# Optimization experiments

Measured on AMD Instinct MI355X. Metric: run time of the kernel, lower is better.

Reference implementation:

```python
import jax, jax.numpy as jnp
import numpy as np

B = 128          # batch
M_SIZE = 32      # mps bond dimension (init kwarg mps_size)
NQ = 16          # num_qubits -> 2**16 basis states


def setup_inputs() -> dict:
    key = jax.random.key(0)
    ks = jax.random.split(key, 4)
    def lin(k, out_d, in_d):
        return jax.random.normal(k, (out_d, in_d), jnp.float32) * (1.0 / np.sqrt(in_d))
    mat = M_SIZE * M_SIZE
    return {
        "x": jax.random.normal(ks[0], (B, 4), jnp.float32),
        "W1": lin(ks[1], 1024, 4),        "b1": jnp.zeros((1024,), jnp.float32),
        "W2": lin(ks[2], 32, 1024),       "b2": jnp.zeros((32,), jnp.float32),
        "W3": lin(ks[3], 2 * mat, 32),    "b3": jnp.zeros((2 * mat,), jnp.float32),
        "num_qubits": NQ,
    }


def _chain_products(M, k):
    """M: [2, B, m, m] site matrices (index 0 = spin_up, 1 = spin_down).
    Returns [2**k, B, m, m]: matrix products A_{s1} @ ... @ A_{sk} for every
    length-k bit string s, ordered as ascending binary (MSB = first/leftmost site),
    matching seq_gen's enumeration order."""
    arr = M
    for _ in range(k - 1):  # recursive doubling over sites (static small loop)
        arr = jnp.einsum('sbij,tbjk->stbik', arr, M)
        arr = arr.reshape((-1,) + M.shape[1:])
    return arr


def reference(x, W1, b1, W2, b2, W3, b3, num_qubits):
    # Encoder MLP (dropout is identity in eval mode)
    h = jax.nn.relu(x @ W1.T + b1)
    h = jax.nn.relu(h @ W2.T + b2)
    e = h @ W3.T + b3                         # [B, 2*m*m]
    m = int(np.sqrt(e.shape[-1] // 2))
    # view(-1, 2, m, m); split dim=1 -> spin_up = [:,0], spin_down = [:,1]
    Ms = e.reshape(-1, 2, m, m).transpose(1, 0, 2, 3)   # [2, B, m, m]
    # Decode: coeff(state) = trace(prod of site matrices). Split the chain in
    # two halves; trace(L_s @ R_t) = sum_ij L[s,i,j] * R[t,j,i].
    k1 = num_qubits // 2
    k2 = num_qubits - k1
    L = _chain_products(Ms, k1)               # [2^k1, B, m, m]
    R = _chain_products(Ms, k2)               # [2^k2, B, m, m]
    coeffs = jnp.einsum('sbij,tbji->stb', L, R)   # [2^k1, 2^k2, B]
    gs = coeffs.reshape(-1, coeffs.shape[-1]).T   # [B, 2^n], binary-ascending order
    return gs / jnp.linalg.norm(gs, axis=1, keepdims=True)
```

## Files before the change

kernel.cpp:

```cpp
#include <hip/hip_runtime.h>
#include <hip/hip_bf16.h>
#include <math.h>

#define BDIM 128

typedef short sh8 __attribute__((ext_vector_type(8)));
typedef __bf16 bf8 __attribute__((ext_vector_type(8)));
typedef float f32x4 __attribute__((ext_vector_type(4)));

__device__ inline float bf2f(unsigned short u) {
    union { unsigned int i; float f; } v; v.i = ((unsigned int)u) << 16; return v.f;
}
__device__ inline unsigned short f2bf(float f) {
    union { unsigned int i; float f; } v; v.f = f;
    unsigned int x = v.i;
    return (unsigned short)((x + 0x7FFFu + ((x >> 16) & 1u)) >> 16);
}

__device__ inline sh8 xshuf(sh8 v, int u) {
    switch (u & 7) {
    case 0: return v;
    case 1: return __builtin_shufflevector(v,v,1,0,3,2,5,4,7,6);
    case 2: return __builtin_shufflevector(v,v,2,3,0,1,6,7,4,5);
    case 3: return __builtin_shufflevector(v,v,3,2,1,0,7,6,5,4);
    case 4: return __builtin_shufflevector(v,v,4,5,6,7,0,1,2,3);
    case 5: return __builtin_shufflevector(v,v,5,4,7,6,1,0,3,2);
    case 6: return __builtin_shufflevector(v,v,6,7,4,5,2,3,0,1);
    default: return __builtin_shufflevector(v,v,7,6,5,4,3,2,1,0);
    }
}

__global__ __launch_bounds__(256) void mlp_kernel(
    const float* __restrict__ x,
    const float* __restrict__ W1, const float* __restrict__ b1,
    const float* __restrict__ W2, const float* __restrict__ b2,
    const float* __restrict__ W3, const float* __restrict__ b3,
    float* __restrict__ Mout)
{
    __shared__ float h1[1024];
    __shared__ float part[8][33];
    __shared__ float h2[32];
    int b = blockIdx.x, t = threadIdx.x;
    float x0 = x[b*4+0], x1 = x[b*4+1], x2 = x[b*4+2], x3 = x[b*4+3];
#pragma unroll
    for (int q = 0; q < 4; ++q) {
        int j = t + 256*q;
        float4 w = *(const float4*)(W1 + (size_t)j*4);
        float v = x0*w.x + x1*w.y + x2*w.z + x3*w.w + b1[j];
        h1[j] = v > 0.f ? v : 0.f;
    }
    __syncthreads();
    {
        int o = t & 31, chunk = t >> 5;
        const float* w2r = W2 + (size_t)o*1024 + chunk*128;
        const float* h1r = h1 + chunk*128;
        float s = 0.f;
#pragma unroll
        for (int k = 0; k < 128; k += 4) {
            float4 w = *(const float4*)(w2r + k);
            s += h1r[k]*w.x + h1r[k+1]*w.y + h1r[k+2]*w.z + h1r[k+3]*w.w;
        }
        part[chunk][o] = s;
    }
    __syncthreads();
    if (t < 32) {
        float s = b2[t];
#pragma unroll
        for (int c = 0; c < 8; ++c) s += part[c][t];
        h2[t] = s > 0.f ? s : 0.f;
    }
    __syncthreads();
#pragma unroll
    for (int q = 0; q < 8; ++q) {
        int j = t + 256*q;
        const float* w3r = W3 + (size_t)j*32;
        float s = b3[j];
#pragma unroll
        for (int i = 0; i < 32; i += 4) {
            float4 w = *(const float4*)(w3r + i);
            s += h2[i]*w.x + h2[i+1]*w.y + h2[i+2]*w.z + h2[i+3]*w.w;
        }
        Mout[(size_t)b*2048 + j] = s;
    }
}

__global__ __launch_bounds__(256) void small_chain(
    const float* __restrict__ Mb, float* __restrict__ P4n)
{
    int b = blockIdx.x, t = threadIdx.x;
    __shared__ float aT[2][32][36], an[2][32][36];
    __shared__ float p2T[4][32][36], p2n[4][32][36];
    int w = t >> 6, l = t & 63;
    {
        const float* src = Mb + (size_t)b*2048;
#pragma unroll
        for (int r = 0; r < 2; ++r) {
            int e = t*4 + r*1024;
            float4 v = *(const float4*)(src + e);
            int mat = e >> 10, off = e & 1023;
            int row = off >> 5, c = off & 31;
            *(float4*)&an[mat][row][c] = v;
            aT[mat][c+0][row] = v.x; aT[mat][c+1][row] = v.y;
            aT[mat][c+2][row] = v.z; aT[mat][c+3][row] = v.w;
        }
    }
    __syncthreads();
    int r0 = (l >> 3) << 2, c0 = (l & 7) << 2;
    {
        float acc[4][4] = {};
#pragma unroll 8
        for (int kk = 0; kk < 32; ++kk) {
            float a[4], bb[4];
            *(float4*)a  = *(const float4*)&aT[w>>1][kk][r0];
            *(float4*)bb = *(const float4*)&an[w&1][kk][c0];
#pragma unroll
            for (int i = 0; i < 4; ++i)
#pragma unroll
                for (int j = 0; j < 4; ++j)
                    acc[i][j] += a[i]*bb[j];
        }
#pragma unroll
        for (int i = 0; i < 4; ++i)
#pragma unroll
            for (int j = 0; j < 4; ++j) {
                p2n[w][r0+i][c0+j] = acc[i][j];
                p2T[w][c0+j][r0+i] = acc[i][j];
            }
    }
    __syncthreads();
#pragma unroll
    for (int it = 0; it < 4; ++it) {
        int u = (w << 2) | it;
        float acc[4][4] = {};
#pragma unroll 8
        for (int kk = 0; kk < 32; ++kk) {
            float a[4], bb[4];
            *(float4*)a  = *(const float4*)&p2T[w][kk][r0];
            *(float4*)bb = *(const float4*)&p2n[it][kk][c0];
#pragma unroll
            for (int i = 0; i < 4; ++i)
#pragma unroll
                for (int j = 0; j < 4; ++j)
                    acc[i][j] += a[i]*bb[j];
        }
        float* dst = P4n + ((size_t)b*16 + u)*1024;
#pragma unroll
        for (int i = 0; i < 4; ++i)
            *(float4*)(dst + (r0+i)*32 + c0) =
                make_float4(acc[i][0], acc[i][1], acc[i][2], acc[i][3]);
    }
}

__global__ __launch_bounds__(256) void ll_kernel(
    const float* __restrict__ P4n, unsigned short* __restrict__ LL)
{
    int b = blockIdx.y;
    int q0 = blockIdx.x * 4;
    int hi = q0 >> 4;
    __shared__ float parT[32][36];
    __shared__ float mm[4][32][36];
    __shared__ unsigned short stage[4][1024];
    int t = threadIdx.x, w = t >> 6, l = t & 63;
    {
        const float* src = P4n + ((size_t)b*16 + hi)*1024;
        int e = t*4;
        float4 v = *(const float4*)(src + e);
        int row = e >> 5, c = e & 31;
        parT[c+0][row] = v.x; parT[c+1][row] = v.y;
        parT[c+2][row] = v.z; parT[c+3][row] = v.w;
    }
    {
        const float* src = P4n + ((size_t)b*16 + ((q0 & 15) | w))*1024;
#pragma unroll
        for (int r = 0; r < 4; ++r) {
            int e = r*256 + l*4;
            *(float4*)&mm[w][e>>5][e&31] = *(const float4*)(src + e);
        }
    }
    __syncthreads();
    int r0 = (l >> 3) << 2, c0 = (l & 7) << 2;
    float acc[4][4] = {};
#pragma unroll 8
    for (int kk = 0; kk < 32; ++kk) {
        float a[4], bb[4];
        *(float4*)a  = *(const float4*)&parT[kk][r0];
        *(float4*)bb = *(const float4*)&mm[w][kk][c0];
#pragma unroll
        for (int i = 0; i < 4; ++i)
#pragma unroll
            for (int j = 0; j < 4; ++j)
                acc[i][j] += a[i]*bb[j];
    }
#pragma unroll
    for (int i = 0; i < 4; ++i)
#pragma unroll
        for (int j = 0; j < 4; ++j) {
            int r = r0 + i, c = c0 + j;
            stage[w][((r ^ c) << 5) | c] = f2bf(acc[i][j]);
        }
    __syncthreads();
    unsigned short* dst = LL + ((size_t)b*256 + q0)*1024;
    const uint4* s4 = (const uint4*)&stage[0][0];
    uint4* d4 = (uint4*)dst;
    d4[t] = s4[t];
    d4[t + 256] = s4[t + 256];
}

__global__ __launch_bounds__(256) void pair_gemm_mfma(
    const unsigned short* __restrict__ LL,
    float* __restrict__ out, float* __restrict__ norm2)
{
    int b = blockIdx.y;
    int ti = blockIdx.x >> 1, tj = blockIdx.x & 1;
    const unsigned short* Ab = LL + (size_t)b*262144 + (size_t)ti*131072;
    const unsigned short* Bb = LL + (size_t)b*262144 + (size_t)tj*131072;
    __shared__ __align__(16) unsigned short As[2][128][40];
    __shared__ __align__(16) unsigned short Bs[2][128][40];
    __shared__ float wsum[4];
    int t = threadIdx.x;
    int w = t >> 6, l = t & 63;
    int row0 = t >> 2;
    int j8 = (t & 3) * 8;
    int wm = (w >> 1) * 64, wn = (w & 1) * 64;
    int lr = l & 15, lg = l >> 4;

    const unsigned short* Ar0 = Ab + (size_t)row0*1024;
    const unsigned short* Ar1 = Ab + (size_t)(row0+64)*1024;
    const unsigned short* Br0 = Bb + (size_t)row0*1024;
    const unsigned short* Br1 = Bb + (size_t)(row0+64)*1024;

    f32x4 acc[4][4] = {};
    sh8 ra0, ra1, rb0, rb1;

    ra0 = *(const sh8*)(Ar0 + j8);
    ra1 = *(const sh8*)(Ar1 + j8);
    rb0 = *(const sh8*)(Br0 + j8);
    rb1 = *(const sh8*)(Br1 + j8);
    *(sh8*)&As[0][row0][j8]    = ra0;
    *(sh8*)&As[0][row0+64][j8] = ra1;
    *(sh8*)&Bs[0][row0][j8]    = rb0;
    *(sh8*)&Bs[0][row0+64][j8] = rb1;
    __syncthreads();

#pragma unroll
    for (int d = 0; d < 32; ++d) {
        int cur = d & 1, nxt = cur ^ 1;
        int dn = d + 1;
        if (dn < 32) {
            int aoff = dn*32 + j8;
            int boff = dn*32 + (j8 ^ ((dn >> 3) << 3));
            ra0 = *(const sh8*)(Ar0 + aoff);
            ra1 = *(const sh8*)(Ar1 + aoff);
            rb0 = *(const sh8*)(Br0 + boff);
            rb1 = *(const sh8*)(Br1 + boff);
        }
        bf8 av[4], bv[4];
#pragma unroll
        for (int m = 0; m < 4; ++m) {
            av[m] = __builtin_bit_cast(bf8, *(const sh8*)&As[cur][wm + m*16 + lr][lg*8]);
            bv[m] = __builtin_bit_cast(bf8, *(const sh8*)&Bs[cur][wn + m*16 + lr][lg*8]);
        }
#pragma unroll
        for (int m = 0; m < 4; ++m)
#pragma unroll
            for (int n = 0; n < 4; ++n)
                acc[m][n] = __builtin_amdgcn_mfma_f32_16x16x32_bf16(av[m], bv[n], acc[m][n], 0, 0, 0);
        if (dn < 32) {
            int u = dn & 7;
            *(sh8*)&As[nxt][row0][j8]    = ra0;
            *(sh8*)&As[nxt][row0+64][j8] = ra1;
            *(sh8*)&Bs[nxt][row0][j8]    = xshuf(rb0, u);
            *(sh8*)&Bs[nxt][row0+64][j8] = xshuf(rb1, u);
        }
        __syncthreads();
    }

    float ss = 0.f;
    size_t ob = (size_t)b*65536;
#pragma unroll
    for (int m = 0; m < 4; ++m) {
#pragma unroll
        for (int n = 0; n < 4; ++n) {
            f32x4 v = acc[m][n];
            int s0 = ti*128 + wm + m*16 + lg*4;
            int t0 = tj*128 + wn + n*16 + lr;
            float* op = out + ob + (size_t)s0*256 + t0;
#pragma unroll
            for (int r = 0; r < 4; ++r) {
                op[r*256] = v[r];
                ss += v[r]*v[r];
            }
        }
    }
#pragma unroll
    for (int o = 1; o < 64; o <<= 1) ss += __shfl_xor(ss, o);
    if (l == 0) wsum[w] = ss;
    __syncthreads();
    if (t == 0) atomicAdd(norm2 + b, wsum[0]+wsum[1]+wsum[2]+wsum[3]);
}

__global__ __launch_bounds__(256) void scale_kernel(
    float* __restrict__ out, const float* __restrict__ norm2)
{
    size_t i = (size_t)blockIdx.x * 256 + threadIdx.x;
    int b = (int)(i >> 14);
    float s = rsqrtf(norm2[b]);
    float4 v = ((const float4*)out)[i];
    v.x *= s; v.y *= s; v.z *= s; v.w *= s;
    ((float4*)out)[i] = v;
}

extern "C" void kernel_launch(void* const* d_in, const int* in_sizes, int n_in,
                              void* d_out, int out_size, void* d_ws, size_t ws_size,
                              hipStream_t stream)
{
    (void)in_sizes; (void)n_in;
    const float* x  = (const float*)d_in[0];
    const float* W1 = (const float*)d_in[1];
    const float* b1 = (const float*)d_in[2];
    const float* W2 = (const float*)d_in[3];
    const float* b2 = (const float*)d_in[4];
    const float* W3 = (const float*)d_in[5];
    const float* b3 = (const float*)d_in[6];
    float* out = (float*)d_out;

    char* W = (char*)d_ws;
    const size_t MB = 1024*1024;
    unsigned short* LL = (unsigned short*)(W + 0);
    float* P4 = (float*)(W + 64*MB);
    float* Mb = (float*)(W + 72*MB);
    float* nrm = (float*)(W + 73*MB);
    const size_t NEED = 73*MB + 512;
    if (ws_size < NEED) {
        hipMemsetAsync(d_out, 0, (size_t)out_size * sizeof(float), stream);
        return;
    }

    hipMemsetAsync(nrm, 0, BDIM*sizeof(float), stream);
    mlp_kernel<<<BDIM, 256, 0, stream>>>(x, W1, b1, W2, b2, W3, b3, Mb);
    small_chain<<<BDIM, 256, 0, stream>>>(Mb, P4);
    ll_kernel<<<dim3(64, BDIM), 256, 0, stream>>>(P4, LL);
    pair_gemm_mfma<<<dim3(4, BDIM), 256, 0, stream>>>(LL, out, nrm);
    scale_kernel<<<8192, 256, 0, stream>>>(out, nrm);
}
```

Baseline: 183.5 us.

## Fuse encoder with chain products and compute level-8 products via bf16 MFMA

Merges the MLP encoder and the 2/4-site chain product kernels into one kernel, keeping site matrices in shared memory and folding the norm memset into it. The 4-site products are written as bf16 in both normal and transposed layouts. The 8-site product stage is rewritten as a bf16 MFMA kernel in which each block computes 16 outputs instead of 4. This cuts launches and global round trips, but adds bf16 rounding one stage earlier, which may reduce accuracy.

```diff
diff --git a/kernel.cpp b/kernel.cpp
--- a/kernel.cpp
+++ b/kernel.cpp
@@ -30,17 +30,21 @@
     }
 }
 
-__global__ __launch_bounds__(256) void mlp_kernel(
+__global__ __launch_bounds__(256) void enc_fused(
     const float* __restrict__ x,
     const float* __restrict__ W1, const float* __restrict__ b1,
     const float* __restrict__ W2, const float* __restrict__ b2,
     const float* __restrict__ W3, const float* __restrict__ b3,
-    float* __restrict__ Mout)
+    unsigned short* __restrict__ P4n, unsigned short* __restrict__ P4t,
+    float* __restrict__ nrm)
 {
     __shared__ float h1[1024];
     __shared__ float part[8][33];
     __shared__ float h2[32];
+    __shared__ float aT[2][32][36], an[2][32][36];
+    __shared__ float p2T[4][32][36], p2n[4][32][36];
     int b = blockIdx.x, t = threadIdx.x;
+    if (t == 0) nrm[b] = 0.f;
     float x0 = x[b*4+0], x1 = x[b*4+1], x2 = x[b*4+2], x3 = x[b*4+3];
 #pragma unroll
     for (int q = 0; q < 4; ++q) {
@@ -80,31 +84,13 @@
             float4 w = *(const float4*)(w3r + i);
             s += h2[i]*w.x + h2[i+1]*w.y + h2[i+2]*w.z + h2[i+3]*w.w;
         }
-        Mout[(size_t)b*2048 + j] = s;
-    }
-}
-
-__global__ __launch_bounds__(256) void small_chain(
-    const float* __restrict__ Mb, float* __restrict__ P4n)
-{
-    int b = blockIdx.x, t = threadIdx.x;
-    __shared__ float aT[2][32][36], an[2][32][36];
-    __shared__ float p2T[4][32][36], p2n[4][32][36];
+        int spin = j >> 10, off = j & 1023;
+        int row = off >> 5, c = off & 31;
+        an[spin][row][c] = s;
+        aT[spin][c][row] = s;
+    }
+    __syncthreads();
     int w = t >> 6, l = t & 63;
-    {
-        const float* src = Mb + (size_t)b*2048;
-#pragma unroll
-        for (int r = 0; r < 2; ++r) {
-            int e = t*4 + r*1024;
-            float4 v = *(const float4*)(src + e);
-            int mat = e >> 10, off = e & 1023;
-            int row = off >> 5, c = off & 31;
-            *(float4*)&an[mat][row][c] = v;
-            aT[mat][c+0][row] = v.x; aT[mat][c+1][row] = v.y;
-            aT[mat][c+2][row] = v.z; aT[mat][c+3][row] = v.w;
-        }
-    }
-    __syncthreads();
     int r0 = (l >> 3) << 2, c0 = (l & 7) << 2;
     {
         float acc[4][4] = {};
@@ -143,67 +129,86 @@
                 for (int j = 0; j < 4; ++j)
                     acc[i][j] += a[i]*bb[j];
         }
-        float* dst = P4n + ((size_t)b*16 + u)*1024;
-#pragma unroll
-        for (int i = 0; i < 4; ++i)
-            *(float4*)(dst + (r0+i)*32 + c0) =
-                make_float4(acc[i][0], acc[i][1], acc[i][2], acc[i][3]);
-    }
-}
-
-__global__ __launch_bounds__(256) void ll_kernel(
-    const float* __restrict__ P4n, unsigned short* __restrict__ LL)
-{
-    int b = blockIdx.y;
-    int q0 = blockIdx.x * 4;
-    int hi = q0 >> 4;
-    __shared__ float parT[32][36];
-    __shared__ float mm[4][32][36];
-    __shared__ unsigned short stage[4][1024];
-    int t = threadIdx.x, w = t >> 6, l = t & 63;
+        unsigned short* dstN = P4n + ((size_t)b*16 + u)*1024;
+        unsigned short* dstT = P4t + ((size_t)b*16 + u)*1024;
+#pragma unroll
+        for (int i = 0; i < 4; ++i) {
+            ushort4 v; v.x = f2bf(acc[i][0]); v.y = f2bf(acc[i][1]);
+            v.z = f2bf(acc[i][2]); v.w = f2bf(acc[i][3]);
+            *(ushort4*)(dstN + (r0+i)*32 + c0) = v;
+        }
+#pragma unroll
+        for (int j = 0; j < 4; ++j) {
+            ushort4 v; v.x = f2bf(acc[0][j]); v.y = f2bf(acc[1][j]);
+            v.z = f2bf(acc[2][j]); v.w = f2bf(acc[3][j]);
+            *(ushort4*)(dstT + (c0+j)*32 + r0) = v;
+        }
+    }
+}
+
+__global__ __launch_bounds__(256) void ll_mfma(
+    const unsigned short* __restrict__ P4n, const unsigned short* __restrict__ P4t,
+    unsigned short* __restrict__ LL)
+{
+    int hi = blockIdx.x, b = blockIdx.y;
+    __shared__ __align__(16) unsigned short As[32][40];
+    __shared__ __align__(16) unsigned short Bs[512][40];
+    __shared__ __align__(16) unsigned short outst[16][1024];
+    int t = threadIdx.x;
+    int w = t >> 6, l = t & 63;
+    int lr = l & 15, lg = l >> 4;
+    int wn = w * 128;
+
     {
-        const float* src = P4n + ((size_t)b*16 + hi)*1024;
-        int e = t*4;
-        float4 v = *(const float4*)(src + e);
-        int row = e >> 5, c = e & 31;
-        parT[c+0][row] = v.x; parT[c+1][row] = v.y;
-        parT[c+2][row] = v.z; parT[c+3][row] = v.w;
-    }
-    {
-        const float* src = P4n + ((size_t)b*16 + ((q0 & 15) | w))*1024;
-#pragma unroll
-        for (int r = 0; r < 4; ++r) {
-            int e = r*256 + l*4;
-            *(float4*)&mm[w][e>>5][e&31] = *(const float4*)(src + e);
-        }
-    }
-    __syncthreads();
-    int r0 = (l >> 3) << 2, c0 = (l & 7) << 2;
-    float acc[4][4] = {};
-#pragma unroll 8
-    for (int kk = 0; kk < 32; ++kk) {
-        float a[4], bb[4];
-        *(float4*)a  = *(const float4*)&parT[kk][r0];
-        *(float4*)bb = *(const float4*)&mm[w][kk][c0];
-#pragma unroll
-        for (int i = 0; i < 4; ++i)
-#pragma unroll
-            for (int j = 0; j < 4; ++j)
-                acc[i][j] += a[i]*bb[j];
-    }
-#pragma unroll
-    for (int i = 0; i < 4; ++i)
-#pragma unroll
-        for (int j = 0; j < 4; ++j) {
-            int r = r0 + i, c = c0 + j;
-            stage[w][((r ^ c) << 5) | c] = f2bf(acc[i][j]);
-        }
-    __syncthreads();
-    unsigned short* dst = LL + ((size_t)b*256 + q0)*1024;
-    const uint4* s4 = (const uint4*)&stage[0][0];
+        if (t < 128) {
+            int i = t >> 2, k8 = (t & 3) * 8;
+            *(sh8*)&As[i][k8] = *(const sh8*)(P4n + ((size_t)b*16 + hi)*1024 + i*32 + k8);
+        }
+#pragma unroll
+        for (int rep = 0; rep < 8; ++rep) {
+            int flat = rep*256 + t;
+            int n = flat >> 2, k8 = (flat & 3) * 8;
+            *(sh8*)&Bs[n][k8] =
+                *(const sh8*)(P4t + ((size_t)b*16 + (n >> 5))*1024 + (n & 31)*32 + k8);
+        }
+    }
+    __syncthreads();
+
+    f32x4 acc[2][8] = {};
+    bf8 av[2], bv[8];
+#pragma unroll
+    for (int m = 0; m < 2; ++m)
+        av[m] = __builtin_bit_cast(bf8, *(const sh8*)&As[m*16 + lr][lg*8]);
+#pragma unroll
+    for (int n = 0; n < 8; ++n)
+        bv[n] = __builtin_bit_cast(bf8, *(const sh8*)&Bs[wn + n*16 + lr][lg*8]);
+#pragma unroll
+    for (int m = 0; m < 2; ++m)
+#pragma unroll
+        for (int n = 0; n < 8; ++n)
+            acc[m][n] = __builtin_amdgcn_mfma_f32_16x16x32_bf16(av[m], bv[n], acc[m][n], 0, 0, 0);
+    __syncthreads();
+
+#pragma unroll
+    for (int m = 0; m < 2; ++m)
+#pragma unroll
+        for (int n = 0; n < 8; ++n) {
+            f32x4 v = acc[m][n];
+            int col = wn + n*16 + lr;
+            int qlo = col >> 5, j = col & 31;
+#pragma unroll
+            for (int r = 0; r < 4; ++r) {
+                int i = m*16 + lg*4 + r;
+                outst[qlo][((i ^ j) << 5) | j] = f2bf(v[r]);
+            }
+        }
+    __syncthreads();
+    unsigned short* dst = LL + ((size_t)b*256 + hi*16)*1024;
+    const uint4* s4 = (const uint4*)&outst[0][0];
     uint4* d4 = (uint4*)dst;
-    d4[t] = s4[t];
-    d4[t + 256] = s4[t + 256];
+#pragma unroll
+    for (int rep = 0; rep < 8; ++rep)
+        d4[rep*256 + t] = s4[rep*256 + t];
 }
 
 __global__ __launch_bounds__(256) void pair_gemm_mfma(
@@ -326,20 +331,18 @@
 
     char* W = (char*)d_ws;
     const size_t MB = 1024*1024;
-    unsigned short* LL = (unsigned short*)(W + 0);
-    float* P4 = (float*)(W + 64*MB);
-    float* Mb = (float*)(W + 72*MB);
-    float* nrm = (float*)(W + 73*MB);
-    const size_t NEED = 73*MB + 512;
+    unsigned short* LL  = (unsigned short*)(W + 0);
+    unsigned short* P4n = (unsigned short*)(W + 64*MB);
+    unsigned short* P4t = (unsigned short*)(W + 68*MB);
+    float* nrm = (float*)(W + 72*MB);
+    const size_t NEED = 72*MB + 512;
     if (ws_size < NEED) {
         hipMemsetAsync(d_out, 0, (size_t)out_size * sizeof(float), stream);
         return;
     }
 
-    hipMemsetAsync(nrm, 0, BDIM*sizeof(float), stream);
-    mlp_kernel<<<BDIM, 256, 0, stream>>>(x, W1, b1, W2, b2, W3, b3, Mb);
-    small_chain<<<BDIM, 256, 0, stream>>>(Mb, P4);
-    ll_kernel<<<dim3(64, BDIM), 256, 0, stream>>>(P4, LL);
+    enc_fused<<<BDIM, 256, 0, stream>>>(x, W1, b1, W2, b2, W3, b3, P4n, P4t, nrm);
+    ll_mfma<<<dim3(16, BDIM), 256, 0, stream>>>(P4n, P4t, LL);
     pair_gemm_mfma<<<dim3(4, BDIM), 256, 0, stream>>>(LL, out, nrm);
     scale_kernel<<<8192, 256, 0, stream>>>(out, nrm);
 }
```

Result: faster. 161.2 us (-12.2%).
